# Optimization experiments

Measured on AMD Instinct MI355X. Metric: run time of the kernel, lower is better.

## Reference

```python
import jax, jax.numpy as jnp
import numpy as np

B, S, D = 4, 2048, 768
H = 12
DH = D // H  # 64
DF = 2048
THETA = 10000.0
EPS = 1e-5


def setup_inputs() -> dict:
    key = jax.random.key(0)
    ks = jax.random.split(key, 8)
    sc = 0.02  # keep activations numerically tame
    return {
        "x": jax.random.normal(ks[0], (B, S, D), jnp.float32),
        "ln1_w": jnp.ones((D,), jnp.float32),
        "ln2_w": jnp.ones((D,), jnp.float32),
        "p_q": jax.random.normal(ks[1], (D, D), jnp.float32) * sc,
        "p_k": jax.random.normal(ks[2], (D, D), jnp.float32) * sc,
        "p_v": jax.random.normal(ks[3], (D, D), jnp.float32) * sc,
        "p_o": jax.random.normal(ks[4], (D, D), jnp.float32) * sc,
        "w1": jax.random.normal(ks[5], (DF, D), jnp.float32) * sc,
        "w2": jax.random.normal(ks[6], (D, DF), jnp.float32) * sc,
        "w3": jax.random.normal(ks[7], (DF, D), jnp.float32) * sc,
    }


def _rmsnorm(x, w):
    # matches torch: fp32 compute, mean-square + eps
    rms = jnp.sqrt(jnp.mean(x * x, axis=-1, keepdims=True) + EPS)
    return x / rms * w


def _rope(t):
    # t: [B, H, S, DH]; rotation per RoPE matrix: pairs (2k, 2k+1)
    pos = jnp.arange(S, dtype=jnp.float32)[:, None]            # [S,1]
    k = jnp.arange(DH // 2, dtype=jnp.float32)[None, :]        # [1,DH/2]
    ang = pos / (THETA ** (2.0 * k / DH))                      # [S,DH/2]
    cos, sin = jnp.cos(ang), jnp.sin(ang)
    t2 = t.reshape(*t.shape[:-1], DH // 2, 2)
    x0, x1 = t2[..., 0], t2[..., 1]
    o0 = cos * x0 - sin * x1
    o1 = sin * x0 + cos * x1
    return jnp.stack([o0, o1], axis=-1).reshape(t.shape)


def reference(x, ln1_w, ln2_w, p_q, p_k, p_v, p_o, w1, w2, w3):
    # --- attention sublayer ---
    h = _rmsnorm(x, ln1_w)                                     # [B,S,D]
    Wq = p_q.reshape(H, DH, D)
    Wk = p_k.reshape(H, DH, D)
    Wv = p_v.reshape(H, DH, D)
    q = _rope(jnp.einsum('bsd,hed->bhse', h, Wq))              # [B,H,S,DH]
    k = _rope(jnp.einsum('bsd,hed->bhse', h, Wk))
    v = jnp.einsum('bsd,hed->bhse', h, Wv)
    scores = jnp.einsum('bhqe,bhke->bhqk', q, k)               # [B,H,S,S]
    mask = jnp.tril(jnp.ones((S, S), bool))
    scores = jnp.where(mask, scores, -jnp.inf)
    attn = jax.nn.softmax(scores / jnp.sqrt(jnp.float32(DH)), axis=-1)
    ctx = jnp.einsum('bhqk,bhke->bhqe', attn, v)               # [B,H,S,DH]
    ctx = jnp.transpose(ctx, (0, 2, 1, 3)).reshape(B, S, D)    # [B,S,D]
    x = x + ctx @ p_o.T
    # --- SwiGLU FFN sublayer ---
    h2 = _rmsnorm(x, ln2_w)
    u1 = h2 @ w1.T
    u1 = u1 * jax.nn.sigmoid(u1)                               # SiLU
    u3 = h2 @ w3.T
    x = x + (u1 * u3) @ w2.T
    return x
```

## Files before the change

kernel.cpp:

```cpp
#include <hip/hip_runtime.h>
#include <stdint.h>

#define B_  4
#define S_  2048
#define D_  768
#define H_  12
#define DH_ 64
#define DF_ 2048
#define M_  (B_*S_)
#define NQKV 2304
#define N13  4096

typedef __attribute__((ext_vector_type(8))) short bf16x8;
typedef __attribute__((ext_vector_type(4))) short bf16x4;
typedef __attribute__((ext_vector_type(4))) float f32x4;
typedef unsigned short u16;

#if !defined(__HIP_DEVICE_COMPILE__)
  #define MFMA_K16(A,B,C) (C)
#elif __has_builtin(__builtin_amdgcn_mfma_f32_16x16x16_bf16)
  #define MFMA_K16(A,B,C) __builtin_amdgcn_mfma_f32_16x16x16_bf16((A),(B),(C),0,0,0)
#else
  #define MFMA_K16(A,B,C) __builtin_amdgcn_mfma_f32_16x16x16bf16_1k((A),(B),(C),0,0,0)
#endif

__device__ __forceinline__ float bf2f(u16 v) {
  union { uint32_t u; float f; } x; x.u = ((uint32_t)v) << 16; return x.f;
}
__device__ __forceinline__ u16 f2bf(float f) {
  union { float f; uint32_t u; } x; x.f = f;
  uint32_t r = x.u + 0x7FFFu + ((x.u >> 16) & 1u);
  return (u16)(r >> 16);
}
__device__ __forceinline__ void gl_lds16(const u16* g, u16* l) {
  __builtin_amdgcn_global_load_lds((const __attribute__((address_space(1))) uint32_t*)g,
                                   (__attribute__((address_space(3))) uint32_t*)l, 16, 0, 0);
}

__global__ __launch_bounds__(256) void cast_bf16_kernel(const float* __restrict__ in,
                                                        u16* __restrict__ out, int n4) {
  int i = blockIdx.x * 256 + threadIdx.x;
  if (i >= n4) return;
  float4 v = ((const float4*)in)[i];
  ushort4 o;
  o.x = f2bf(v.x); o.y = f2bf(v.y); o.z = f2bf(v.z); o.w = f2bf(v.w);
  ((ushort4*)out)[i] = o;
}

__global__ __launch_bounds__(192) void cast_w13_kernel(const float* __restrict__ w1,
                                                       const float* __restrict__ w3,
                                                       u16* __restrict__ out) {
  int j = blockIdx.x, which = blockIdx.y;
  const float* src = (which ? w3 : w1) + (size_t)j * D_;
  int fr = (j >> 4) * 32 + (j & 15) + which * 16;
  u16* dst = out + (size_t)fr * D_;
  int t = threadIdx.x;
  float4 v = ((const float4*)src)[t];
  ushort4 o;
  o.x = f2bf(v.x); o.y = f2bf(v.y); o.z = f2bf(v.z); o.w = f2bf(v.w);
  ((ushort4*)dst)[t] = o;
}

__global__ __launch_bounds__(256) void rmsnorm_kernel(const float* __restrict__ x,
                                                      const float* __restrict__ w,
                                                      u16* __restrict__ out) {
  int row = blockIdx.x, tid = threadIdx.x;
  const float* xr = x + (size_t)row * D_;
  float v0 = xr[tid], v1 = xr[tid + 256], v2 = xr[tid + 512];
  float ss = v0 * v0 + v1 * v1 + v2 * v2;
  #pragma unroll
  for (int m = 32; m >= 1; m >>= 1) ss += __shfl_xor(ss, m, 64);
  __shared__ float red[4];
  if ((tid & 63) == 0) red[tid >> 6] = ss;
  __syncthreads();
  float tot = red[0] + red[1] + red[2] + red[3];
  float r = rsqrtf(tot * (1.0f / D_) + 1e-5f);
  u16* o = out + (size_t)row * D_;
  o[tid]       = f2bf(v0 * r * w[tid]);
  o[tid + 256] = f2bf(v1 * r * w[tid + 256]);
  o[tid + 512] = f2bf(v2 * r * w[tid + 512]);
}

template<int MT, int EPI>
__global__ __launch_bounds__(256) void gemm_bt_kernel(const u16* __restrict__ A,
                                                      const u16* __restrict__ W,
                                                      void* __restrict__ Cout,
                                                      const float* __restrict__ res,
                                                      u16* __restrict__ vTout,
                                                      int K, int N) {
  __shared__ __align__(16) u16 As[MT * 64];
  __shared__ __align__(16) u16 Bs[128 * 64];
  constexpr int MI = MT / 32;
  int tid = threadIdx.x;
  int wave = tid >> 6, lane = tid & 63;
  int quad = lane >> 4, l16 = lane & 15;
  int wr = (wave >> 1) * (MT / 2), wc = (wave & 1) * 64;
  int m0 = blockIdx.y * MT, n0 = blockIdx.x * 128;
  f32x4 acc[MI][4] = {};
  for (int kt = 0; kt < K; kt += 64) {
    __syncthreads();
    #pragma unroll
    for (int i = 0; i < MT / 32; ++i) {
      int idx = i * 256 + tid;
      int r = idx >> 3, c = idx & 7;
      gl_lds16(&A[(size_t)(m0 + r) * K + kt + ((c ^ (r & 7)) * 8)], &As[(i * 256 + wave * 64) * 8]);
    }
    #pragma unroll
    for (int i = 0; i < 4; ++i) {
      int idx = i * 256 + tid;
      int r = idx >> 3, c = idx & 7;
      gl_lds16(&W[(size_t)(n0 + r) * K + kt + ((c ^ (r & 7)) * 8)], &Bs[(i * 256 + wave * 64) * 8]);
    }
    __syncthreads();
    #pragma unroll
    for (int ks = 0; ks < 2; ++ks) {
      bf16x8 af[MI], bf[4];
      int sw = ((ks * 4 + quad) ^ (l16 & 7)) * 8;
      #pragma unroll
      for (int t = 0; t < MI; ++t)
        af[t] = *(const bf16x8*)&As[(wr + t * 16 + l16) * 64 + sw];
      #pragma unroll
      for (int t = 0; t < 4; ++t)
        bf[t] = *(const bf16x8*)&Bs[(wc + t * 16 + l16) * 64 + sw];
      #pragma unroll
      for (int mt = 0; mt < MI; ++mt)
        #pragma unroll
        for (int nt = 0; nt < 4; ++nt)
          acc[mt][nt] = __builtin_amdgcn_mfma_f32_16x16x32_bf16(af[mt], bf[nt], acc[mt][nt], 0, 0, 0);
    }
  }
  #pragma unroll
  for (int mt = 0; mt < MI; ++mt) {
    if (EPI == 3 && n0 + wc >= 1536) {
      int sbase = m0 + wr + mt * 16 + quad * 4;
      int b = sbase >> 11, s = sbase & 2047;
      #pragma unroll
      for (int nt = 0; nt < 4; ++nt) {
        int vcol = n0 + wc + nt * 16 + l16 - 1536;
        int h = vcol >> 6, dh = vcol & 63;
        ushort4 o;
        o.x = f2bf(acc[mt][nt][0]); o.y = f2bf(acc[mt][nt][1]);
        o.z = f2bf(acc[mt][nt][2]); o.w = f2bf(acc[mt][nt][3]);
        *(ushort4*)&vTout[((size_t)(b * H_ + h) * 64 + dh) * (size_t)S_ + s] = o;
      }
    } else {
      #pragma unroll
      for (int r = 0; r < 4; ++r) {
        int gr = m0 + wr + mt * 16 + quad * 4 + r;
        if (EPI == 2) {
          #pragma unroll
          for (int np = 0; np < 2; ++np) {
            float u1v = acc[mt][np * 2][r], u3v = acc[mt][np * 2 + 1][r];
            float sg = 1.0f / (1.0f + __builtin_amdgcn_exp2f(-u1v * 1.44269504f));
            float g = u1v * sg * u3v;
            int gc = (n0 >> 1) + (wave & 1) * 32 + np * 16 + l16;
            ((u16*)Cout)[(size_t)gr * (N >> 1) + gc] = f2bf(g);
          }
        } else {
          #pragma unroll
          for (int nt = 0; nt < 4; ++nt) {
            int gc = n0 + wc + nt * 16 + l16;
            size_t off = (size_t)gr * N + gc;
            float vv = acc[mt][nt][r];
            if (EPI == 1) ((float*)Cout)[off] = vv + res[off];
            else          ((u16*)Cout)[off] = f2bf(vv);
          }
        }
      }
    }
  }
}

__global__ __launch_bounds__(384) void rope_kernel(u16* __restrict__ qkv) {
  int row = blockIdx.x;
  int pos = row & (S_ - 1);
  int t = threadIdx.x;
  int h = t >> 5, kk = t & 31;
  float ang = (float)pos * exp2f(-0.41524101186092035f * (float)kk);
  float c = cosf(ang), s = sinf(ang);
  size_t idx = (size_t)row * NQKV + h * DH_ + 2 * kk;
  const float qs = 0.125f * 1.44269504088896f;
  float q0 = bf2f(qkv[idx]), q1 = bf2f(qkv[idx + 1]);
  qkv[idx]     = f2bf((c * q0 - s * q1) * qs);
  qkv[idx + 1] = f2bf((s * q0 + c * q1) * qs);
  size_t kb = idx + 768;
  float k0 = bf2f(qkv[kb]), k1 = bf2f(qkv[kb + 1]);
  qkv[kb]     = f2bf(c * k0 - s * k1);
  qkv[kb + 1] = f2bf(s * k0 + c * k1);
}

__global__ __launch_bounds__(256, 4) void attn_kernel(const u16* __restrict__ qkv,
                                                      const u16* __restrict__ vT,
                                                      u16* __restrict__ ctx) {
  __shared__ __align__(16) u16 Ks[128 * 64];
  __shared__ __align__(16) u16 Vt[64 * 128];
  int bh = blockIdx.x;
  int qt = 15 - blockIdx.y;
  int b = bh / H_, h = bh % H_;
  const u16* qbase = qkv + (size_t)b * S_ * NQKV + h * DH_;
  const u16* kbase = qbase + 768;
  const u16* vtb   = vT + (size_t)bh * 64 * S_;
  int tid = threadIdx.x, wave = tid >> 6, lane = tid & 63;
  int quad = lane >> 4, l16 = lane & 15;
  const float MFIX = 12.0f;

  bf16x8 qf[2][2];
  #pragma unroll
  for (int mt = 0; mt < 2; ++mt) {
    int qrow = qt * 128 + wave * 32 + mt * 16 + l16;
    qf[mt][0] = *(const bf16x8*)&qbase[(size_t)qrow * NQKV + quad * 8];
    qf[mt][1] = *(const bf16x8*)&qbase[(size_t)qrow * NQKV + 32 + quad * 8];
  }
  f32x4 oacc[2][4] = {};
  float lsum[2] = {0.f, 0.f};
  int nkt = qt + 1;
  for (int kt = 0; kt < nkt; ++kt) {
    __syncthreads();
    #pragma unroll
    for (int i = 0; i < 4; ++i) {
      int idx = i * 256 + tid;
      int r = idx >> 3, c = idx & 7;
      gl_lds16(&kbase[(size_t)(kt * 128 + r) * NQKV + ((c ^ (r & 7)) * 8)],
               &Ks[(i * 256 + wave * 64) * 8]);
    }
    #pragma unroll
    for (int i = 0; i < 4; ++i) {
      int idx = i * 256 + tid;
      int d = idx >> 4, c16 = idx & 15;
      gl_lds16(&vtb[(size_t)d * S_ + kt * 128 + ((c16 ^ (d & 15)) * 8)],
               &Vt[(i * 256 + wave * 64) * 8]);
    }
    __syncthreads();
    bool diag = (kt == nkt - 1);
    #pragma unroll
    for (int t = 0; t < 8; ++t) {
      if (diag && t > 2 * wave + 1) break;
      f32x4 sc0 = {}, sc1 = {};
      #pragma unroll
      for (int c = 0; c < 2; ++c) {
        bf16x8 kf = *(const bf16x8*)&Ks[(t * 16 + l16) * 64 + (((c * 4 + quad) ^ (l16 & 7)) * 8)];
        sc0 = __builtin_amdgcn_mfma_f32_16x16x32_bf16(kf, qf[0][c], sc0, 0, 0, 0);
        sc1 = __builtin_amdgcn_mfma_f32_16x16x32_bf16(kf, qf[1][c], sc1, 0, 0, 0);
      }
      bf16x4 pf[2];
      #pragma unroll
      for (int mt = 0; mt < 2; ++mt) {
        f32x4 sv = mt ? sc1 : sc0;
        float p[4];
        #pragma unroll
        for (int r = 0; r < 4; ++r) p[r] = __builtin_amdgcn_exp2f(sv[r] - MFIX);
        if (diag) {
          int ql = wave * 32 + mt * 16 + l16;
          #pragma unroll
          for (int r = 0; r < 4; ++r)
            if (t * 16 + quad * 4 + r > ql) p[r] = 0.f;
        }
        lsum[mt] += (p[0] + p[1]) + (p[2] + p[3]);
        uint32_t lo = ((__float_as_uint(p[0]) + 0x8000u) >> 16) |
                      ((__float_as_uint(p[1]) + 0x8000u) & 0xFFFF0000u);
        uint32_t hi = ((__float_as_uint(p[2]) + 0x8000u) >> 16) |
                      ((__float_as_uint(p[3]) + 0x8000u) & 0xFFFF0000u);
        uint2 pk; pk.x = lo; pk.y = hi;
        pf[mt] = *(bf16x4*)&pk;
      }
      #pragma unroll
      for (int n = 0; n < 4; ++n) {
        bf16x4 vf = *(const bf16x4*)&Vt[(n * 16 + l16) * 128 +
                                        (((t * 2 + (quad >> 1)) ^ l16) * 8) + (quad & 1) * 4];
        oacc[0][n] = MFMA_K16(vf, pf[0], oacc[0][n]);
        oacc[1][n] = MFMA_K16(vf, pf[1], oacc[1][n]);
      }
    }
  }
  #pragma unroll
  for (int mt = 0; mt < 2; ++mt) {
    float l = lsum[mt];
    l += __shfl_xor(l, 16, 64);
    l += __shfl_xor(l, 32, 64);
    float inv = 1.0f / l;
    int qrow = qt * 128 + wave * 32 + mt * 16 + l16;
    #pragma unroll
    for (int n = 0; n < 4; ++n) {
      ushort4 o;
      o.x = f2bf(oacc[mt][n][0] * inv);
      o.y = f2bf(oacc[mt][n][1] * inv);
      o.z = f2bf(oacc[mt][n][2] * inv);
      o.w = f2bf(oacc[mt][n][3] * inv);
      *(ushort4*)&ctx[(size_t)(b * S_ + qrow) * D_ + h * DH_ + n * 16 + quad * 4] = o;
    }
  }
}

#define WQKV_OFF 0u
#define W13_OFF  3538944u
#define W2_OFF   9830400u
#define WO_OFF   12976128u
#define HB_OFF   14155776u
#define QKV_OFF  26738688u
#define VT_OFF   64487424u
#define X1_OFF   77070336u
#define G_OFF    102236160u

extern "C" void kernel_launch(void* const* d_in, const int* in_sizes, int n_in,
                              void* d_out, int out_size, void* d_ws, size_t ws_size,
                              hipStream_t stream) {
  const float* x    = (const float*)d_in[0];
  const float* ln1w = (const float*)d_in[1];
  const float* ln2w = (const float*)d_in[2];
  const float* pq   = (const float*)d_in[3];
  const float* pk   = (const float*)d_in[4];
  const float* pv   = (const float*)d_in[5];
  const float* po   = (const float*)d_in[6];
  const float* w1   = (const float*)d_in[7];
  const float* w2   = (const float*)d_in[8];
  const float* w3   = (const float*)d_in[9];
  char* ws = (char*)d_ws;
  u16* wqkv = (u16*)(ws + WQKV_OFF);
  u16* w13b = (u16*)(ws + W13_OFF);
  u16* w2b  = (u16*)(ws + W2_OFF);
  u16* wob  = (u16*)(ws + WO_OFF);
  u16* hb   = (u16*)(ws + HB_OFF);
  u16* qkvb = (u16*)(ws + QKV_OFF);
  u16* vtb  = (u16*)(ws + VT_OFF);
  u16* cb   = (u16*)(ws + HB_OFF);
  float* x1 = (float*)(ws + X1_OFF);
  u16* h2b  = (u16*)(ws + VT_OFF);
  u16* gb   = (u16*)(ws + G_OFF);

  cast_bf16_kernel<<<576, 256, 0, stream>>>(pq, wqkv, 147456);
  cast_bf16_kernel<<<576, 256, 0, stream>>>(pk, wqkv + 589824, 147456);
  cast_bf16_kernel<<<576, 256, 0, stream>>>(pv, wqkv + 1179648, 147456);
  cast_bf16_kernel<<<576, 256, 0, stream>>>(po, wob, 147456);
  cast_bf16_kernel<<<1536, 256, 0, stream>>>(w2, w2b, 393216);
  cast_w13_kernel<<<dim3(2048, 2), 192, 0, stream>>>(w1, w3, w13b);

  rmsnorm_kernel<<<M_, 256, 0, stream>>>(x, ln1w, hb);
  gemm_bt_kernel<128, 3><<<dim3(18, 64), 256, 0, stream>>>(hb, wqkv, qkvb, nullptr, vtb, 768, NQKV);
  rope_kernel<<<M_, 384, 0, stream>>>(qkvb);
  attn_kernel<<<dim3(48, 16), 256, 0, stream>>>(qkvb, vtb, cb);
  gemm_bt_kernel<64, 1><<<dim3(6, 128), 256, 0, stream>>>(cb, wob, x1, x, nullptr, 768, 768);

  rmsnorm_kernel<<<M_, 256, 0, stream>>>(x1, ln2w, h2b);
  gemm_bt_kernel<128, 2><<<dim3(32, 64), 256, 0, stream>>>(h2b, w13b, gb, nullptr, nullptr, 768, N13);
  gemm_bt_kernel<64, 1><<<dim3(6, 128), 256, 0, stream>>>(gb, w2b, (float*)d_out, x1, nullptr, 2048, 768);
}
```

Baseline: 365.2 us.

## Fuse RoPE into QKV GEMM epilogue, stage V transpose via LDS, merge casts

```diff
diff --git a/kernel.cpp b/kernel.cpp
--- a/kernel.cpp
+++ b/kernel.cpp
@@ -37,14 +37,26 @@
                                    (__attribute__((address_space(3))) uint32_t*)l, 16, 0, 0);
 }
 
-__global__ __launch_bounds__(256) void cast_bf16_kernel(const float* __restrict__ in,
-                                                        u16* __restrict__ out, int n4) {
-  int i = blockIdx.x * 256 + threadIdx.x;
-  if (i >= n4) return;
-  float4 v = ((const float4*)in)[i];
+__global__ __launch_bounds__(256) void cast_all_kernel(const float* __restrict__ pq,
+                                                       const float* __restrict__ pk,
+                                                       const float* __restrict__ pv,
+                                                       const float* __restrict__ po,
+                                                       const float* __restrict__ w2,
+                                                       u16* __restrict__ wqkv,
+                                                       u16* __restrict__ wob,
+                                                       u16* __restrict__ w2b) {
+  int bidx = blockIdx.x;
+  const float* src; u16* dst; int off;
+  if (bidx < 576)       { src = pq; dst = wqkv;           off = bidx; }
+  else if (bidx < 1152) { src = pk; dst = wqkv + 589824;  off = bidx - 576; }
+  else if (bidx < 1728) { src = pv; dst = wqkv + 1179648; off = bidx - 1152; }
+  else if (bidx < 2304) { src = po; dst = wob;            off = bidx - 1728; }
+  else                  { src = w2; dst = w2b;            off = bidx - 2304; }
+  int i = off * 256 + threadIdx.x;
+  float4 v = ((const float4*)src)[i];
   ushort4 o;
   o.x = f2bf(v.x); o.y = f2bf(v.y); o.z = f2bf(v.z); o.w = f2bf(v.w);
-  ((ushort4*)out)[i] = o;
+  ((ushort4*)dst)[i] = o;
 }
 
 __global__ __launch_bounds__(192) void cast_w13_kernel(const float* __restrict__ w1,
@@ -88,8 +100,11 @@
                                                       const float* __restrict__ res,
                                                       u16* __restrict__ vTout,
                                                       int K, int N) {
-  __shared__ __align__(16) u16 As[MT * 64];
-  __shared__ __align__(16) u16 Bs[128 * 64];
+  constexpr int ABELEMS = MT * 64 + 128 * 64;
+  constexpr int SMELEMS = (EPI == 3 && 128 * 132 > ABELEMS) ? 128 * 132 : ABELEMS;
+  __shared__ __align__(16) u16 smem[SMELEMS];
+  u16* As = smem;
+  u16* Bs = smem + MT * 64;
   constexpr int MI = MT / 32;
   int tid = threadIdx.x;
   int wave = tid >> 6, lane = tid & 63;
@@ -129,21 +144,60 @@
           acc[mt][nt] = __builtin_amdgcn_mfma_f32_16x16x32_bf16(af[mt], bf[nt], acc[mt][nt], 0, 0, 0);
     }
   }
-  #pragma unroll
-  for (int mt = 0; mt < MI; ++mt) {
-    if (EPI == 3 && n0 + wc >= 1536) {
-      int sbase = m0 + wr + mt * 16 + quad * 4;
-      int b = sbase >> 11, s = sbase & 2047;
+
+  if (EPI == 3 && n0 >= 1536) {
+    __syncthreads();
+    #pragma unroll
+    for (int mt = 0; mt < MI; ++mt) {
+      int sloc = wr + mt * 16 + quad * 4;
       #pragma unroll
       for (int nt = 0; nt < 4; ++nt) {
-        int vcol = n0 + wc + nt * 16 + l16 - 1536;
-        int h = vcol >> 6, dh = vcol & 63;
+        int col = wc + nt * 16 + l16;
         ushort4 o;
         o.x = f2bf(acc[mt][nt][0]); o.y = f2bf(acc[mt][nt][1]);
         o.z = f2bf(acc[mt][nt][2]); o.w = f2bf(acc[mt][nt][3]);
-        *(ushort4*)&vTout[((size_t)(b * H_ + h) * 64 + dh) * (size_t)S_ + s] = o;
-      }
-    } else {
+        *(ushort4*)&smem[col * 132 + sloc] = o;
+      }
+    }
+    __syncthreads();
+    int b = m0 >> 11, sblk = m0 & 2047;
+    #pragma unroll
+    for (int i = 0; i < 8; ++i) {
+      int idx = i * 256 + tid;
+      int row = idx >> 4, c16 = idx & 15;
+      uint4 d = *(const uint4*)&smem[row * 132 + c16 * 8];
+      int vg = n0 - 1536 + row;
+      int h = vg >> 6, dh = vg & 63;
+      *(uint4*)&vTout[((size_t)(b * H_ + h) * 64 + dh) * (size_t)S_ + sblk + c16 * 8] = d;
+    }
+  } else if (EPI == 3) {
+    bool isq = (n0 < 768);
+    float osc = isq ? 0.18033688f : 1.0f;
+    #pragma unroll
+    for (int mt = 0; mt < MI; ++mt) {
+      int r0 = m0 + wr + mt * 16 + quad * 4;
+      int pos0 = r0 & 2047;
+      #pragma unroll
+      for (int nt = 0; nt < 4; ++nt) {
+        int col = n0 + wc + nt * 16 + l16;
+        int kk = (col & 63) >> 1;
+        float freq = exp2f(-0.41524101186092035f * (float)kk);
+        bool odd = (col & 1);
+        #pragma unroll
+        for (int r = 0; r < 4; ++r) {
+          float own = acc[mt][nt][r];
+          float pv = __shfl_xor(own, 1, 64);
+          float ang = (float)(pos0 + r) * freq;
+          float sv, cv;
+          __sincosf(ang, &sv, &cv);
+          float o = odd ? (sv * pv + cv * own) : (cv * own - sv * pv);
+          ((u16*)Cout)[(size_t)(r0 + r) * N + col] = f2bf(o * osc);
+        }
+      }
+    }
+  } else {
+    #pragma unroll
+    for (int mt = 0; mt < MI; ++mt) {
       #pragma unroll
       for (int r = 0; r < 4; ++r) {
         int gr = m0 + wr + mt * 16 + quad * 4 + r;
@@ -169,24 +223,6 @@
       }
     }
   }
-}
-
-__global__ __launch_bounds__(384) void rope_kernel(u16* __restrict__ qkv) {
-  int row = blockIdx.x;
-  int pos = row & (S_ - 1);
-  int t = threadIdx.x;
-  int h = t >> 5, kk = t & 31;
-  float ang = (float)pos * exp2f(-0.41524101186092035f * (float)kk);
-  float c = cosf(ang), s = sinf(ang);
-  size_t idx = (size_t)row * NQKV + h * DH_ + 2 * kk;
-  const float qs = 0.125f * 1.44269504088896f;
-  float q0 = bf2f(qkv[idx]), q1 = bf2f(qkv[idx + 1]);
-  qkv[idx]     = f2bf((c * q0 - s * q1) * qs);
-  qkv[idx + 1] = f2bf((s * q0 + c * q1) * qs);
-  size_t kb = idx + 768;
-  float k0 = bf2f(qkv[kb]), k1 = bf2f(qkv[kb + 1]);
-  qkv[kb]     = f2bf(c * k0 - s * k1);
-  qkv[kb + 1] = f2bf(s * k0 + c * k1);
 }
 
 __global__ __launch_bounds__(256, 4) void attn_kernel(const u16* __restrict__ qkv,
@@ -327,16 +363,11 @@
   u16* h2b  = (u16*)(ws + VT_OFF);
   u16* gb   = (u16*)(ws + G_OFF);
 
-  cast_bf16_kernel<<<576, 256, 0, stream>>>(pq, wqkv, 147456);
-  cast_bf16_kernel<<<576, 256, 0, stream>>>(pk, wqkv + 589824, 147456);
-  cast_bf16_kernel<<<576, 256, 0, stream>>>(pv, wqkv + 1179648, 147456);
-  cast_bf16_kernel<<<576, 256, 0, stream>>>(po, wob, 147456);
-  cast_bf16_kernel<<<1536, 256, 0, stream>>>(w2, w2b, 393216);
+  cast_all_kernel<<<3840, 256, 0, stream>>>(pq, pk, pv, po, w2, wqkv, wob, w2b);
   cast_w13_kernel<<<dim3(2048, 2), 192, 0, stream>>>(w1, w3, w13b);
 
   rmsnorm_kernel<<<M_, 256, 0, stream>>>(x, ln1w, hb);
   gemm_bt_kernel<128, 3><<<dim3(18, 64), 256, 0, stream>>>(hb, wqkv, qkvb, nullptr, vtb, 768, NQKV);
-  rope_kernel<<<M_, 384, 0, stream>>>(qkvb);
   attn_kernel<<<dim3(48, 16), 256, 0, stream>>>(qkvb, vtb, cb);
   gemm_bt_kernel<64, 1><<<dim3(6, 128), 256, 0, stream>>>(cb, wob, x1, x, nullptr, 768, 768);
 
```

Result: no change. 361.9 us (-0.9%).
